# Optimization experiments

Hardware: AMD Instinct MI355X
Metric: run time of the kernel (lower is better)

Reference implementation:

```python
import jax, jax.numpy as jnp
import numpy as np

N_HEADS = 16
D_MODEL = 1024
D_K = 64
D_V = 64
LN_EPS = 1e-6


def setup_inputs() -> dict:
    key = jax.random.key(0)
    ks = jax.random.split(key, 16)
    B, L, D = 4, 512, D_MODEL
    s = 1.0 / np.sqrt(D)
    return {
        "q": jax.random.normal(ks[0], (B, L, D), jnp.float32),
        "k": jax.random.normal(ks[1], (B, L, D), jnp.float32),
        "v": jax.random.normal(ks[2], (B, L, D), jnp.float32),
        "bias": jax.random.normal(ks[3], (B, N_HEADS, L, L), jnp.float32),
        "graph_attn_bias": jax.random.normal(ks[4], (B, N_HEADS, L, L), jnp.float32),
        # projection weights stored as [in, out] (math-equivalent to torch Linear)
        "wq": jax.random.normal(ks[5], (D, N_HEADS * D_K), jnp.float32) * s,
        "bq": jnp.zeros((N_HEADS * D_K,), jnp.float32),
        "wk": jax.random.normal(ks[6], (D, N_HEADS * D_K), jnp.float32) * s,
        "bk": jnp.zeros((N_HEADS * D_K,), jnp.float32),
        "wv": jax.random.normal(ks[7], (D, N_HEADS * D_V), jnp.float32) * s,
        "bv": jnp.zeros((N_HEADS * D_V,), jnp.float32),
        "wo": jax.random.normal(ks[8], (N_HEADS * D_V, D), jnp.float32) * s,
        "bo": jnp.zeros((D,), jnp.float32),
        "ln_g": jnp.ones((D,), jnp.float32),
        "ln_b": jnp.zeros((D,), jnp.float32),
    }


def reference(q, k, v, bias, graph_attn_bias, wq, bq, wk, bk, wv, bv, wo, bo, ln_g, ln_b):
    B, Lq, D = q.shape
    H, dk, dv = N_HEADS, D_K, D_V
    residual = q
    # fused QKV projections, split heads -> [B, H, L, d]
    qh = (q @ wq + bq).reshape(B, Lq, H, dk).transpose(0, 2, 1, 3)
    kh = (k @ wk + bk).reshape(B, k.shape[1], H, dk).transpose(0, 2, 1, 3)
    vh = (v @ wv + bv).reshape(B, v.shape[1], H, dv).transpose(0, 2, 1, 3)
    # graph scaled dot-product attention: scores + mask bias + structural bias
    scores = jnp.einsum("bhqd,bhkd->bhqk", qh / np.sqrt(dk).astype(qh.dtype), kh)
    scores = scores + bias + graph_attn_bias
    weights = jax.nn.softmax(scores, axis=-1)
    ctx = jnp.einsum("bhqk,bhkd->bhqd", weights, vh)  # [B,H,Lq,dv]
    ctx = ctx.transpose(0, 2, 1, 3).reshape(B, Lq, H * dv)
    out = ctx @ wo + bo + residual
    # LayerNorm(eps=1e-6)
    mu = jnp.mean(out, axis=-1, keepdims=True)
    var = jnp.var(out, axis=-1, keepdims=True)
    out = (out - mu) * jax.lax.rsqrt(var + LN_EPS) * ln_g + ln_b
    return out
```

## Files before the change

kernel.cpp:

```cpp
#include <hip/hip_runtime.h>

#define D_MODEL 1024
#define N_HEADS 16
#define DK 64
#define LSEQ 512
#define BATCH 4
#define M_ROWS (BATCH * LSEQ)

typedef unsigned short ushort_t;
typedef __attribute__((ext_vector_type(8))) short short8;
typedef __attribute__((ext_vector_type(4))) float floatx4;

__device__ __forceinline__ float bf2f(unsigned short u) {
    return __uint_as_float(((unsigned int)u) << 16);
}
__device__ __forceinline__ unsigned short f2bf(float f) {
    unsigned int u = __float_as_uint(f);
    u += 0x7fffu + ((u >> 16) & 1u);
    return (unsigned short)(u >> 16);
}

__global__ __launch_bounds__(256) void cast3_kernel(
    const float* __restrict__ a, const float* __restrict__ b,
    const float* __restrict__ c, ushort_t* __restrict__ oa,
    ushort_t* __restrict__ ob, ushort_t* __restrict__ oc, int n)
{
    const float* src = (blockIdx.y == 0) ? a : (blockIdx.y == 1) ? b : c;
    ushort_t* dst = (blockIdx.y == 0) ? oa : (blockIdx.y == 1) ? ob : oc;
    int i = (blockIdx.x * 256 + threadIdx.x) * 4;
    if (i + 3 < n) {
        float4 v = *(const float4*)(src + i);
        ushort4 o = make_ushort4(f2bf(v.x), f2bf(v.y), f2bf(v.z), f2bf(v.w));
        *(ushort4*)(dst + i) = o;
    }
}

__global__ __launch_bounds__(256) void transpose4_kernel(
    const float* __restrict__ w0, const float* __restrict__ w1,
    const float* __restrict__ w2, const float* __restrict__ w3,
    ushort_t* __restrict__ o0, ushort_t* __restrict__ o1,
    ushort_t* __restrict__ o2, ushort_t* __restrict__ o3)
{
    __shared__ float tile[32][33];
    const float* W = (blockIdx.z == 0) ? w0 : (blockIdx.z == 1) ? w1
                   : (blockIdx.z == 2) ? w2 : w3;
    ushort_t* O = (blockIdx.z == 0) ? o0 : (blockIdx.z == 1) ? o1
                : (blockIdx.z == 2) ? o2 : o3;
    const int tx = threadIdx.x & 31;
    const int ty = threadIdx.x >> 5;
    const int kbase = blockIdx.y * 32;
    const int nbase = blockIdx.x * 32;
    #pragma unroll
    for (int j = 0; j < 4; ++j)
        tile[ty + 8 * j][tx] = W[(size_t)(kbase + ty + 8 * j) * 1024 + nbase + tx];
    __syncthreads();
    #pragma unroll
    for (int j = 0; j < 4; ++j) {
        int n = nbase + ty + 8 * j;
        O[(size_t)n * 1024 + kbase + tx] = f2bf(tile[tx][ty + 8 * j]);
    }
}

template <bool OUT_BF16, bool ADD_BVEC, bool ADD_RES>
__device__ __forceinline__ void gemm_bt_body(
    const ushort_t* __restrict__ A, const ushort_t* __restrict__ Bt,
    const float* __restrict__ bvec, const float* __restrict__ res,
    void* __restrict__ outp, int N, int K, int kStart, int kEnd,
    int rowBase, int colBase, ushort_t* As, ushort_t* Bs)
{
    const int tid = threadIdx.x;
    const int l = tid & 63;
    const int w = tid >> 6;
    const int wave_m = w >> 1;
    const int wave_n = w & 1;

    const int srow8 = l >> 3;
    const int cgl = ((l & 7) + srow8) & 7;
    const ushort_t* gA0 = A  + (size_t)(rowBase + w * 16 + 0 + srow8) * K + cgl * 8;
    const ushort_t* gA1 = A  + (size_t)(rowBase + w * 16 + 8 + srow8) * K + cgl * 8;
    const ushort_t* gB0 = Bt + (size_t)(colBase + w * 16 + 0 + srow8) * K + cgl * 8;
    const ushort_t* gB1 = Bt + (size_t)(colBase + w * 16 + 8 + srow8) * K + cgl * 8;
    ushort_t* lA0 = As + w * 1024;
    ushort_t* lA1 = As + w * 1024 + 512;
    ushort_t* lB0 = Bs + w * 1024;
    ushort_t* lB1 = Bs + w * 1024 + 512;

    floatx4 acc[2][2];
    #pragma unroll
    for (int i = 0; i < 2; ++i)
        #pragma unroll
        for (int j = 0; j < 2; ++j)
            acc[i][j] = (floatx4){0.f, 0.f, 0.f, 0.f};

    const int fm = l & 15;
    const int fg = l >> 4;

    for (int k0 = kStart; k0 < kEnd; k0 += 64) {
        __builtin_amdgcn_global_load_lds(
            (const __attribute__((address_space(1))) void*)(gA0 + k0),
            (__attribute__((address_space(3))) void*)lA0, 16, 0, 0);
        __builtin_amdgcn_global_load_lds(
            (const __attribute__((address_space(1))) void*)(gA1 + k0),
            (__attribute__((address_space(3))) void*)lA1, 16, 0, 0);
        __builtin_amdgcn_global_load_lds(
            (const __attribute__((address_space(1))) void*)(gB0 + k0),
            (__attribute__((address_space(3))) void*)lB0, 16, 0, 0);
        __builtin_amdgcn_global_load_lds(
            (const __attribute__((address_space(1))) void*)(gB1 + k0),
            (__attribute__((address_space(3))) void*)lB1, 16, 0, 0);
        __syncthreads();

        short8 afrag[2][2], bfrag[2][2];
        #pragma unroll
        for (int mi = 0; mi < 2; ++mi)
            #pragma unroll
            for (int kt = 0; kt < 2; ++kt) {
                int p = ((kt * 4 + fg) - fm) & 7;
                afrag[mi][kt] = *(const short8*)
                    &As[(wave_m * 32 + mi * 16 + fm) * 64 + p * 8];
            }
        #pragma unroll
        for (int ni = 0; ni < 2; ++ni)
            #pragma unroll
            for (int kt = 0; kt < 2; ++kt) {
                int p = ((kt * 4 + fg) - fm) & 7;
                bfrag[ni][kt] = *(const short8*)
                    &Bs[(wave_n * 32 + ni * 16 + fm) * 64 + p * 8];
            }

        #pragma unroll
        for (int kt = 0; kt < 2; ++kt)
            #pragma unroll
            for (int mi = 0; mi < 2; ++mi)
                #pragma unroll
                for (int ni = 0; ni < 2; ++ni)
                    acc[mi][ni] = __builtin_amdgcn_mfma_f32_16x16x32_bf16(
                        afrag[mi][kt], bfrag[ni][kt], acc[mi][ni], 0, 0, 0);
        __syncthreads();
    }

    const int crow0 = rowBase + wave_m * 32 + fg * 4;
    const int ccol0 = colBase + wave_n * 32 + fm;
    #pragma unroll
    for (int mi = 0; mi < 2; ++mi) {
        #pragma unroll
        for (int ni = 0; ni < 2; ++ni) {
            const int col = ccol0 + ni * 16;
            const float bb = ADD_BVEC ? bvec[col] : 0.f;
            #pragma unroll
            for (int r = 0; r < 4; ++r) {
                const int row = crow0 + mi * 16 + r;
                float v = acc[mi][ni][r] + bb;
                if (ADD_RES) v += res[(size_t)row * N + col];
                if (OUT_BF16)
                    ((ushort_t*)outp)[(size_t)row * N + col] = f2bf(v);
                else
                    ((float*)outp)[(size_t)row * N + col] = v;
            }
        }
    }
}

__global__ __launch_bounds__(256) void gemm_qkv(
    const ushort_t* a0, const ushort_t* a1, const ushort_t* a2,
    const ushort_t* t0, const ushort_t* t1, const ushort_t* t2,
    const float* b0, const float* b1, const float* b2,
    ushort_t* o0, ushort_t* o1, ushort_t* o2)
{
    __shared__ ushort_t As[64 * 64];
    __shared__ ushort_t Bs[64 * 64];
    const int z = blockIdx.z;
    const ushort_t* A  = (z == 0) ? a0 : (z == 1) ? a1 : a2;
    const ushort_t* Bt = (z == 0) ? t0 : (z == 1) ? t1 : t2;
    const float* bv    = (z == 0) ? b0 : (z == 1) ? b1 : b2;
    ushort_t* o        = (z == 0) ? o0 : (z == 1) ? o1 : o2;
    gemm_bt_body<true, true, false>(A, Bt, bv, nullptr, o, D_MODEL, D_MODEL,
                                    0, D_MODEL,
                                    blockIdx.y * 64, blockIdx.x * 64, As, Bs);
}

__global__ __launch_bounds__(256) void gemm_out(
    const ushort_t* __restrict__ A, const ushort_t* __restrict__ Bt,
    const float* __restrict__ bvec, const float* __restrict__ res,
    float* __restrict__ out0, float* __restrict__ out1)
{
    __shared__ ushort_t As[64 * 64];
    __shared__ ushort_t Bs[64 * 64];
    if (blockIdx.z == 0)
        gemm_bt_body<false, true, true>(A, Bt, bvec, res, out0, D_MODEL,
                                        D_MODEL, 0, 512,
                                        blockIdx.y * 64, blockIdx.x * 64, As, Bs);
    else
        gemm_bt_body<false, false, false>(A, Bt, nullptr, nullptr, out1, D_MODEL,
                                          D_MODEL, 512, 1024,
                                          blockIdx.y * 64, blockIdx.x * 64, As, Bs);
}

__global__ __launch_bounds__(256, 4) void attn_mfma(
    const ushort_t* __restrict__ qh, const ushort_t* __restrict__ kh,
    const ushort_t* __restrict__ vh, const float* __restrict__ bias,
    const float* __restrict__ gbias, ushort_t* __restrict__ ctx)
{
    __shared__ __attribute__((aligned(16))) ushort_t Qs[16 * 72];
    __shared__ __attribute__((aligned(16))) ushort_t P[16 * 520];
    __shared__ float Vt[64 * 36];
    __shared__ float redm[4][16];
    __shared__ float reds[4][16];

    const int tid = threadIdx.x;
    const int l = tid & 63;
    const int w = tid >> 6;
    const int m = l & 15;
    const int g = l >> 4;

    const int bh = blockIdx.y;
    const int h = bh & (N_HEADS - 1);
    const int b = bh >> 4;
    const int q0 = blockIdx.x * 16;

    const ushort_t* Qg = qh + ((size_t)(b * LSEQ + q0)) * D_MODEL + h * DK;
    const ushort_t* Kg = kh + ((size_t)(b * LSEQ)) * D_MODEL + h * DK;
    const ushort_t* Vg = vh + ((size_t)(b * LSEQ)) * D_MODEL + h * DK;

    if (tid < 128) {
        int row = tid >> 3, seg = tid & 7;
        short8 t = *(const short8*)(Qg + (size_t)row * D_MODEL + seg * 8);
        *(short8*)&Qs[row * 72 + seg * 8] = t;
    }
    __syncthreads();

    short8 aq0 = *(const short8*)&Qs[m * 72 + g * 8];
    short8 aq1 = *(const short8*)&Qs[m * 72 + g * 8 + 32];

    floatx4 acc[8];
    #pragma unroll
    for (int it = 0; it < 8; ++it) {
        const int kb = it * 64 + w * 16;
        const ushort_t* kr = Kg + (size_t)(kb + m) * D_MODEL + g * 8;
        short8 bk0 = *(const short8*)kr;
        short8 bk1 = *(const short8*)(kr + 32);
        floatx4 a = (floatx4){0.f, 0.f, 0.f, 0.f};
        a = __builtin_amdgcn_mfma_f32_16x16x32_bf16(aq0, bk0, a, 0, 0, 0);
        a = __builtin_amdgcn_mfma_f32_16x16x32_bf16(aq1, bk1, a, 0, 0, 0);
        acc[it] = a;
    }

    const float* bp = bias  + ((size_t)bh * LSEQ + q0) * LSEQ + w * 16 + m;
    const float* gp = gbias + ((size_t)bh * LSEQ + q0) * LSEQ + w * 16 + m;
    float bsum[8][4];
    #pragma unroll
    for (int it = 0; it < 8; ++it)
        #pragma unroll
        for (int r = 0; r < 4; ++r) {
            const size_t off = (size_t)(g * 4 + r) * LSEQ + it * 64;
            bsum[it][r] = bp[off] + gp[off];
        }
    #pragma unroll
    for (int it = 0; it < 8; ++it)
        #pragma unroll
        for (int r = 0; r < 4; ++r)
            acc[it][r] = acc[it][r] * 0.125f + bsum[it][r];

    float mx[4];
    #pragma unroll
    for (int r = 0; r < 4; ++r) {
        float pm = fmaxf(
            fmaxf(fmaxf(acc[0][r], acc[1][r]), fmaxf(acc[2][r], acc[3][r])),
            fmaxf(fmaxf(acc[4][r], acc[5][r]), fmaxf(acc[6][r], acc[7][r])));
        #pragma unroll
        for (int d = 1; d < 16; d <<= 1)
            pm = fmaxf(pm, __shfl_xor(pm, d, 64));
        mx[r] = pm;
    }
    if (m == 0) {
        #pragma unroll
        for (int r = 0; r < 4; ++r) redm[w][g * 4 + r] = mx[r];
    }
    __syncthreads();
    #pragma unroll
    for (int r = 0; r < 4; ++r)
        mx[r] = fmaxf(fmaxf(redm[0][g * 4 + r], redm[1][g * 4 + r]),
                      fmaxf(redm[2][g * 4 + r], redm[3][g * 4 + r]));

    float sm[4] = {0.f, 0.f, 0.f, 0.f};
    #pragma unroll
    for (int it = 0; it < 8; ++it)
        #pragma unroll
        for (int r = 0; r < 4; ++r) {
            float e = __expf(acc[it][r] - mx[r]);
            sm[r] += e;
            P[(g * 4 + r) * 520 + it * 64 + w * 16 + m] = f2bf(e);
        }
    #pragma unroll
    for (int r = 0; r < 4; ++r) {
        #pragma unroll
        for (int d = 1; d < 16; d <<= 1)
            sm[r] += __shfl_xor(sm[r], d, 64);
    }
    if (m == 0) {
        #pragma unroll
        for (int r = 0; r < 4; ++r) reds[w][g * 4 + r] = sm[r];
    }
    __syncthreads();
    float rinv[4];
    #pragma unroll
    for (int r = 0; r < 4; ++r)
        rinv[r] = 1.0f / (reds[0][g * 4 + r] + reds[1][g * 4 + r] +
                          reds[2][g * 4 + r] + reds[3][g * 4 + r]);

    floatx4 oacc = (floatx4){0.f, 0.f, 0.f, 0.f};
    const unsigned* VtD = (const unsigned*)Vt;

    for (int vt = 0; vt < 8; ++vt) {
        const int kv0 = vt * 64;
        __syncthreads();
        {
            const int kp = tid & 31, dg = tid >> 5;
            const ushort_t* vr = Vg + (size_t)(kv0 + 2 * kp) * D_MODEL + dg * 8;
            short8 r0 = *(const short8*)vr;
            short8 r1 = *(const short8*)(vr + D_MODEL);
            unsigned* vtp = (unsigned*)Vt;
            #pragma unroll
            for (int i = 0; i < 8; ++i) {
                unsigned dwv = (unsigned)(ushort_t)r0[i]
                             | ((unsigned)(ushort_t)r1[i] << 16);
                vtp[(dg * 8 + i) * 36 + kp] = dwv;
            }
        }
        __syncthreads();
        #pragma unroll
        for (int kt = 0; kt < 2; ++kt) {
            short8 pf = *(const short8*)&P[(size_t)m * 520 + kv0 + kt * 32 + g * 8];
            short8 vf = *(const short8*)&VtD[(w * 16 + m) * 36 + kt * 16 + g * 4];
            oacc = __builtin_amdgcn_mfma_f32_16x16x32_bf16(pf, vf, oacc, 0, 0, 0);
        }
    }

    {
        const int qrow0 = g * 4;
        const int dcol = w * 16 + m;
        ushort_t* cp = ctx + ((size_t)(b * LSEQ + q0 + qrow0)) * D_MODEL + h * DK + dcol;
        #pragma unroll
        for (int r = 0; r < 4; ++r)
            cp[(size_t)r * D_MODEL] = f2bf(oacc[r] * rinv[r]);
    }
}

__global__ __launch_bounds__(256) void ln_kernel(
    float* __restrict__ x, const float* __restrict__ part2,
    const float* __restrict__ g, const float* __restrict__ beta)
{
    const int row = blockIdx.x;
    float* xr = x + (size_t)row * D_MODEL;
    const float* pr = part2 + (size_t)row * D_MODEL;
    const int tid = threadIdx.x;

    float v[4];
    float s = 0.f, sq = 0.f;
    #pragma unroll
    for (int j = 0; j < 4; ++j) {
        v[j] = xr[tid + 256 * j] + pr[tid + 256 * j];
        s += v[j];
        sq += v[j] * v[j];
    }
    __shared__ float rs[256], rq[256];
    rs[tid] = s;
    rq[tid] = sq;
    __syncthreads();
    for (int st = 128; st > 0; st >>= 1) {
        if (tid < st) { rs[tid] += rs[tid + st]; rq[tid] += rq[tid + st]; }
        __syncthreads();
    }
    const float mean = rs[0] * (1.0f / D_MODEL);
    const float var = rq[0] * (1.0f / D_MODEL) - mean * mean;
    const float rinv = rsqrtf(var + 1e-6f);
    #pragma unroll
    for (int j = 0; j < 4; ++j) {
        int n = tid + 256 * j;
        xr[n] = (v[j] - mean) * rinv * g[n] + beta[n];
    }
}

extern "C" void kernel_launch(void* const* d_in, const int* in_sizes, int n_in,
                              void* d_out, int out_size, void* d_ws, size_t ws_size,
                              hipStream_t stream)
{
    const float* q     = (const float*)d_in[0];
    const float* k     = (const float*)d_in[1];
    const float* v     = (const float*)d_in[2];
    const float* bias  = (const float*)d_in[3];
    const float* gbias = (const float*)d_in[4];
    const float* wq    = (const float*)d_in[5];
    const float* bq    = (const float*)d_in[6];
    const float* wk    = (const float*)d_in[7];
    const float* bk    = (const float*)d_in[8];
    const float* wv    = (const float*)d_in[9];
    const float* bv    = (const float*)d_in[10];
    const float* wo    = (const float*)d_in[11];
    const float* bo    = (const float*)d_in[12];
    const float* ln_g  = (const float*)d_in[13];
    const float* ln_b  = (const float*)d_in[14];

    const size_t MB = 1u << 20;
    char* wsb = (char*)d_ws;
    ushort_t* vb   = (ushort_t*)(wsb + 0 * MB);
    ushort_t* wqb  = (ushort_t*)(wsb + 4 * MB);
    ushort_t* wkb  = (ushort_t*)(wsb + 6 * MB);
    ushort_t* wvb  = (ushort_t*)(wsb + 8 * MB);
    ushort_t* wob  = (ushort_t*)(wsb + 10 * MB);
    ushort_t* qhb  = (ushort_t*)(wsb + 12 * MB);
    ushort_t* khb  = (ushort_t*)(wsb + 16 * MB);
    ushort_t* vhb  = (ushort_t*)(wsb + 20 * MB);
    ushort_t* ctxb = (ushort_t*)(wsb + 24 * MB);
    float* out1 = (float*)(wsb + 12 * MB);
    ushort_t* qb = (ushort_t*)d_out;
    ushort_t* kb = (ushort_t*)d_out + (size_t)M_ROWS * D_MODEL;
    float* outp = (float*)d_out;

    const int NELEM = M_ROWS * D_MODEL;

    cast3_kernel<<<dim3(NELEM / 1024, 3), 256, 0, stream>>>(
        q, k, v, qb, kb, vb, NELEM);
    transpose4_kernel<<<dim3(32, 32, 4), 256, 0, stream>>>(
        wq, wk, wv, wo, wqb, wkb, wvb, wob);

    dim3 gqkv(D_MODEL / 64, M_ROWS / 64, 3);
    gemm_qkv<<<gqkv, 256, 0, stream>>>(
        qb, kb, vb, wqb, wkb, wvb, bq, bk, bv, qhb, khb, vhb);

    dim3 ablk(LSEQ / 16, BATCH * N_HEADS);
    attn_mfma<<<ablk, 256, 0, stream>>>(qhb, khb, vhb, bias, gbias, ctxb);

    dim3 gout(D_MODEL / 64, M_ROWS / 64, 2);
    gemm_out<<<gout, 256, 0, stream>>>(ctxb, wob, bo, q, outp, out1);

    ln_kernel<<<M_ROWS, 256, 0, stream>>>(outp, out1, ln_g, ln_b);
}
```

Baseline: 270.2 us.

## Stage bias tiles via async global-to-LDS loads and double-buffer V transposes

The attention kernel now prefetches all K fragments into registers up front. It issues global_load_lds DMA for the bias and graph-bias tiles into a 64KB shared buffer so those loads overlap the QK MFMAs, and then reads the biases from LDS. P and a double-buffered transposed V tile reuse the same shared region, with new strides, and the next V rows are prefetched into registers while MFMAs consume the current buffer, which removes one barrier per iteration. Occupancy drops: launch bounds go from 4 to 2 blocks and LDS use rises to about 67KB per block, so fewer waves are available to hide latency.

```diff
diff --git a/kernel.cpp b/kernel.cpp
--- a/kernel.cpp
+++ b/kernel.cpp
@@ -196,16 +196,24 @@
                                           blockIdx.y * 64, blockIdx.x * 64, As, Bs);
 }
 
-__global__ __launch_bounds__(256, 4) void attn_mfma(
+#define P_STRIDE 536
+#define VT_STRIDE 44
+#define VT_OFF 17408
+#define VT_BYTES 11264
+
+__global__ __launch_bounds__(256, 2) void attn_mfma(
     const ushort_t* __restrict__ qh, const ushort_t* __restrict__ kh,
     const ushort_t* __restrict__ vh, const float* __restrict__ bias,
     const float* __restrict__ gbias, ushort_t* __restrict__ ctx)
 {
+    __shared__ __attribute__((aligned(16))) unsigned char smem[65536];
     __shared__ __attribute__((aligned(16))) ushort_t Qs[16 * 72];
-    __shared__ __attribute__((aligned(16))) ushort_t P[16 * 520];
-    __shared__ float Vt[64 * 36];
     __shared__ float redm[4][16];
     __shared__ float reds[4][16];
+
+    float* biasL  = (float*)smem;
+    float* gbiasL = (float*)(smem + 32768);
+    ushort_t* Pl  = (ushort_t*)smem;
 
     const int tid = threadIdx.x;
     const int l = tid & 63;
@@ -232,34 +240,53 @@
     short8 aq0 = *(const short8*)&Qs[m * 72 + g * 8];
     short8 aq1 = *(const short8*)&Qs[m * 72 + g * 8 + 32];
 
+    short8 bk0[8], bk1[8];
+    #pragma unroll
+    for (int it = 0; it < 8; ++it) {
+        const ushort_t* kr = Kg + (size_t)(it * 64 + w * 16 + m) * D_MODEL + g * 8;
+        bk0[it] = *(const short8*)kr;
+        bk1[it] = *(const short8*)(kr + 32);
+    }
+
+    {
+        const float* bb = bias  + ((size_t)bh * LSEQ + q0) * LSEQ;
+        const float* gb = gbias + ((size_t)bh * LSEQ + q0) * LSEQ;
+        #pragma unroll
+        for (int i = 0; i < 4; ++i) {
+            const int row = w * 4 + i;
+            const size_t roff = (size_t)row * LSEQ;
+            #pragma unroll
+            for (int c = 0; c < 2; ++c) {
+                __builtin_amdgcn_global_load_lds(
+                    (const __attribute__((address_space(1))) void*)(bb + roff + c * 256 + l * 4),
+                    (__attribute__((address_space(3))) void*)(biasL + row * 512 + c * 256),
+                    16, 0, 0);
+                __builtin_amdgcn_global_load_lds(
+                    (const __attribute__((address_space(1))) void*)(gb + roff + c * 256 + l * 4),
+                    (__attribute__((address_space(3))) void*)(gbiasL + row * 512 + c * 256),
+                    16, 0, 0);
+            }
+        }
+    }
+
     floatx4 acc[8];
     #pragma unroll
     for (int it = 0; it < 8; ++it) {
-        const int kb = it * 64 + w * 16;
-        const ushort_t* kr = Kg + (size_t)(kb + m) * D_MODEL + g * 8;
-        short8 bk0 = *(const short8*)kr;
-        short8 bk1 = *(const short8*)(kr + 32);
         floatx4 a = (floatx4){0.f, 0.f, 0.f, 0.f};
-        a = __builtin_amdgcn_mfma_f32_16x16x32_bf16(aq0, bk0, a, 0, 0, 0);
-        a = __builtin_amdgcn_mfma_f32_16x16x32_bf16(aq1, bk1, a, 0, 0, 0);
+        a = __builtin_amdgcn_mfma_f32_16x16x32_bf16(aq0, bk0[it], a, 0, 0, 0);
+        a = __builtin_amdgcn_mfma_f32_16x16x32_bf16(aq1, bk1[it], a, 0, 0, 0);
         acc[it] = a;
     }
 
-    const float* bp = bias  + ((size_t)bh * LSEQ + q0) * LSEQ + w * 16 + m;
-    const float* gp = gbias + ((size_t)bh * LSEQ + q0) * LSEQ + w * 16 + m;
-    float bsum[8][4];
+    __syncthreads();
+
     #pragma unroll
     for (int it = 0; it < 8; ++it)
         #pragma unroll
         for (int r = 0; r < 4; ++r) {
-            const size_t off = (size_t)(g * 4 + r) * LSEQ + it * 64;
-            bsum[it][r] = bp[off] + gp[off];
-        }
-    #pragma unroll
-    for (int it = 0; it < 8; ++it)
-        #pragma unroll
-        for (int r = 0; r < 4; ++r)
-            acc[it][r] = acc[it][r] * 0.125f + bsum[it][r];
+            const int idx = (g * 4 + r) * 512 + it * 64 + w * 16 + m;
+            acc[it][r] = acc[it][r] * 0.125f + (biasL[idx] + gbiasL[idx]);
+        }
 
     float mx[4];
     #pragma unroll
@@ -289,7 +316,7 @@
         for (int r = 0; r < 4; ++r) {
             float e = __expf(acc[it][r] - mx[r]);
             sm[r] += e;
-            P[(g * 4 + r) * 520 + it * 64 + w * 16 + m] = f2bf(e);
+            Pl[(g * 4 + r) * P_STRIDE + it * 64 + w * 16 + m] = f2bf(e);
         }
     #pragma unroll
     for (int r = 0; r < 4; ++r) {
@@ -309,29 +336,29 @@
                           reds[2][g * 4 + r] + reds[3][g * 4 + r]);
 
     floatx4 oacc = (floatx4){0.f, 0.f, 0.f, 0.f};
-    const unsigned* VtD = (const unsigned*)Vt;
-
+    const int kp = tid & 31, dg = tid >> 5;
+    const ushort_t* vb0 = Vg + (size_t)(2 * kp) * D_MODEL + dg * 8;
+    short8 r0 = *(const short8*)vb0;
+    short8 r1 = *(const short8*)(vb0 + D_MODEL);
+
+    #pragma unroll
     for (int vt = 0; vt < 8; ++vt) {
-        const int kv0 = vt * 64;
+        unsigned* vtp = (unsigned*)(smem + VT_OFF + (vt & 1) * VT_BYTES);
+        #pragma unroll
+        for (int i = 0; i < 8; ++i)
+            vtp[(dg * 8 + i) * VT_STRIDE + kp] =
+                (unsigned)(ushort_t)r0[i] | ((unsigned)(ushort_t)r1[i] << 16);
         __syncthreads();
-        {
-            const int kp = tid & 31, dg = tid >> 5;
-            const ushort_t* vr = Vg + (size_t)(kv0 + 2 * kp) * D_MODEL + dg * 8;
-            short8 r0 = *(const short8*)vr;
-            short8 r1 = *(const short8*)(vr + D_MODEL);
-            unsigned* vtp = (unsigned*)Vt;
-            #pragma unroll
-            for (int i = 0; i < 8; ++i) {
-                unsigned dwv = (unsigned)(ushort_t)r0[i]
-                             | ((unsigned)(ushort_t)r1[i] << 16);
-                vtp[(dg * 8 + i) * 36 + kp] = dwv;
-            }
-        }
-        __syncthreads();
+        if (vt < 7) {
+            const ushort_t* vr = vb0 + (size_t)((vt + 1) * 64) * D_MODEL;
+            r0 = *(const short8*)vr;
+            r1 = *(const short8*)(vr + D_MODEL);
+        }
+        const unsigned* VtDb = (const unsigned*)(smem + VT_OFF + (vt & 1) * VT_BYTES);
         #pragma unroll
         for (int kt = 0; kt < 2; ++kt) {
-            short8 pf = *(const short8*)&P[(size_t)m * 520 + kv0 + kt * 32 + g * 8];
-            short8 vf = *(const short8*)&VtD[(w * 16 + m) * 36 + kt * 16 + g * 4];
+            short8 pf = *(const short8*)&Pl[(size_t)m * P_STRIDE + vt * 64 + kt * 32 + g * 8];
+            short8 vf = *(const short8*)&VtDb[(w * 16 + m) * VT_STRIDE + kt * 16 + g * 4];
             oacc = __builtin_amdgcn_mfma_f32_16x16x32_bf16(pf, vf, oacc, 0, 0, 0);
         }
     }
```

Measured after the change: 273.1 us. About the same (+1.1%).

## Write V projection pre-transposed per head and drop in-kernel V transpose

Applied to the files above, without the earlier changes.

The QKV GEMM epilogue now writes the V projection in a per-(batch, head) transposed layout [d][L]. The attention kernel can then load V fragments directly from global memory, removing the per-tile shared-memory transpose and its two barriers per iteration. The attention kernel also raises its occupancy hint to 5 blocks per unit and reduces unrolling of the score and PV loops to 2 to save registers. The trade-off is that the PV loop now issues uncached global loads for V, and the QK loop exposes more load latency.

```diff
diff --git a/kernel.cpp b/kernel.cpp
--- a/kernel.cpp
+++ b/kernel.cpp
@@ -61,7 +61,7 @@
     }
 }
 
-template <bool OUT_BF16, bool ADD_BVEC, bool ADD_RES>
+template <bool OUT_BF16, bool ADD_BVEC, bool ADD_RES, bool OUT_VT>
 __device__ __forceinline__ void gemm_bt_body(
     const ushort_t* __restrict__ A, const ushort_t* __restrict__ Bt,
     const float* __restrict__ bvec, const float* __restrict__ res,
@@ -147,15 +147,27 @@
         for (int ni = 0; ni < 2; ++ni) {
             const int col = ccol0 + ni * 16;
             const float bb = ADD_BVEC ? bvec[col] : 0.f;
-            #pragma unroll
-            for (int r = 0; r < 4; ++r) {
-                const int row = crow0 + mi * 16 + r;
-                float v = acc[mi][ni][r] + bb;
-                if (ADD_RES) v += res[(size_t)row * N + col];
-                if (OUT_BF16)
-                    ((ushort_t*)outp)[(size_t)row * N + col] = f2bf(v);
-                else
-                    ((float*)outp)[(size_t)row * N + col] = v;
+            if (OUT_VT) {
+                const int row0 = crow0 + mi * 16;
+                ushort4 pk;
+                pk.x = f2bf(acc[mi][ni][0] + bb);
+                pk.y = f2bf(acc[mi][ni][1] + bb);
+                pk.z = f2bf(acc[mi][ni][2] + bb);
+                pk.w = f2bf(acc[mi][ni][3] + bb);
+                const size_t base =
+                    ((size_t)((row0 >> 9) * 16 + (col >> 6)) * 64 + (col & 63)) * 512;
+                *(ushort4*)&((ushort_t*)outp)[base + (row0 & 511)] = pk;
+            } else {
+                #pragma unroll
+                for (int r = 0; r < 4; ++r) {
+                    const int row = crow0 + mi * 16 + r;
+                    float v = acc[mi][ni][r] + bb;
+                    if (ADD_RES) v += res[(size_t)row * N + col];
+                    if (OUT_BF16)
+                        ((ushort_t*)outp)[(size_t)row * N + col] = f2bf(v);
+                    else
+                        ((float*)outp)[(size_t)row * N + col] = v;
+                }
             }
         }
     }
@@ -170,13 +182,19 @@
     __shared__ ushort_t As[64 * 64];
     __shared__ ushort_t Bs[64 * 64];
     const int z = blockIdx.z;
-    const ushort_t* A  = (z == 0) ? a0 : (z == 1) ? a1 : a2;
-    const ushort_t* Bt = (z == 0) ? t0 : (z == 1) ? t1 : t2;
-    const float* bv    = (z == 0) ? b0 : (z == 1) ? b1 : b2;
-    ushort_t* o        = (z == 0) ? o0 : (z == 1) ? o1 : o2;
-    gemm_bt_body<true, true, false>(A, Bt, bv, nullptr, o, D_MODEL, D_MODEL,
-                                    0, D_MODEL,
-                                    blockIdx.y * 64, blockIdx.x * 64, As, Bs);
+    if (z == 2) {
+        gemm_bt_body<true, true, false, true>(a2, t2, b2, nullptr, o2, D_MODEL,
+                                              D_MODEL, 0, D_MODEL,
+                                              blockIdx.y * 64, blockIdx.x * 64, As, Bs);
+    } else {
+        const ushort_t* A  = (z == 0) ? a0 : a1;
+        const ushort_t* Bt = (z == 0) ? t0 : t1;
+        const float* bv    = (z == 0) ? b0 : b1;
+        ushort_t* o        = (z == 0) ? o0 : o1;
+        gemm_bt_body<true, true, false, false>(A, Bt, bv, nullptr, o, D_MODEL,
+                                               D_MODEL, 0, D_MODEL,
+                                               blockIdx.y * 64, blockIdx.x * 64, As, Bs);
+    }
 }
 
 __global__ __launch_bounds__(256) void gemm_out(
@@ -187,23 +205,24 @@
     __shared__ ushort_t As[64 * 64];
     __shared__ ushort_t Bs[64 * 64];
     if (blockIdx.z == 0)
-        gemm_bt_body<false, true, true>(A, Bt, bvec, res, out0, D_MODEL,
-                                        D_MODEL, 0, 512,
-                                        blockIdx.y * 64, blockIdx.x * 64, As, Bs);
+        gemm_bt_body<false, true, true, false>(A, Bt, bvec, res, out0, D_MODEL,
+                                               D_MODEL, 0, 512,
+                                               blockIdx.y * 64, blockIdx.x * 64, As, Bs);
     else
-        gemm_bt_body<false, false, false>(A, Bt, nullptr, nullptr, out1, D_MODEL,
-                                          D_MODEL, 512, 1024,
-                                          blockIdx.y * 64, blockIdx.x * 64, As, Bs);
-}
-
-__global__ __launch_bounds__(256, 4) void attn_mfma(
+        gemm_bt_body<false, false, false, false>(A, Bt, nullptr, nullptr, out1, D_MODEL,
+                                                 D_MODEL, 512, 1024,
+                                                 blockIdx.y * 64, blockIdx.x * 64, As, Bs);
+}
+
+#define P_STRIDE 520
+
+__global__ __launch_bounds__(256, 5) void attn_mfma(
     const ushort_t* __restrict__ qh, const ushort_t* __restrict__ kh,
-    const ushort_t* __restrict__ vh, const float* __restrict__ bias,
+    const ushort_t* __restrict__ vt, const float* __restrict__ bias,
     const float* __restrict__ gbias, ushort_t* __restrict__ ctx)
 {
     __shared__ __attribute__((aligned(16))) ushort_t Qs[16 * 72];
-    __shared__ __attribute__((aligned(16))) ushort_t P[16 * 520];
-    __shared__ float Vt[64 * 36];
+    __shared__ __attribute__((aligned(16))) ushort_t P[16 * P_STRIDE];
     __shared__ float redm[4][16];
     __shared__ float reds[4][16];
 
@@ -220,7 +239,7 @@
 
     const ushort_t* Qg = qh + ((size_t)(b * LSEQ + q0)) * D_MODEL + h * DK;
     const ushort_t* Kg = kh + ((size_t)(b * LSEQ)) * D_MODEL + h * DK;
-    const ushort_t* Vg = vh + ((size_t)(b * LSEQ)) * D_MODEL + h * DK;
+    const ushort_t* Vt_g = vt + (size_t)bh * DK * LSEQ;
 
     if (tid < 128) {
         int row = tid >> 3, seg = tid & 7;
@@ -233,7 +252,7 @@
     short8 aq1 = *(const short8*)&Qs[m * 72 + g * 8 + 32];
 
     floatx4 acc[8];
-    #pragma unroll
+    #pragma unroll 2
     for (int it = 0; it < 8; ++it) {
         const int kb = it * 64 + w * 16;
         const ushort_t* kr = Kg + (size_t)(kb + m) * D_MODEL + g * 8;
@@ -289,7 +308,7 @@
         for (int r = 0; r < 4; ++r) {
             float e = __expf(acc[it][r] - mx[r]);
             sm[r] += e;
-            P[(g * 4 + r) * 520 + it * 64 + w * 16 + m] = f2bf(e);
+            P[(g * 4 + r) * P_STRIDE + it * 64 + w * 16 + m] = f2bf(e);
         }
     #pragma unroll
     for (int r = 0; r < 4; ++r) {
@@ -309,29 +328,15 @@
                           reds[2][g * 4 + r] + reds[3][g * 4 + r]);
 
     floatx4 oacc = (floatx4){0.f, 0.f, 0.f, 0.f};
-    const unsigned* VtD = (const unsigned*)Vt;
-
-    for (int vt = 0; vt < 8; ++vt) {
-        const int kv0 = vt * 64;
-        __syncthreads();
-        {
-            const int kp = tid & 31, dg = tid >> 5;
-            const ushort_t* vr = Vg + (size_t)(kv0 + 2 * kp) * D_MODEL + dg * 8;
-            short8 r0 = *(const short8*)vr;
-            short8 r1 = *(const short8*)(vr + D_MODEL);
-            unsigned* vtp = (unsigned*)Vt;
-            #pragma unroll
-            for (int i = 0; i < 8; ++i) {
-                unsigned dwv = (unsigned)(ushort_t)r0[i]
-                             | ((unsigned)(ushort_t)r1[i] << 16);
-                vtp[(dg * 8 + i) * 36 + kp] = dwv;
-            }
-        }
-        __syncthreads();
+    const ushort_t* vrow = Vt_g + (size_t)(w * 16 + m) * LSEQ + g * 8;
+    const ushort_t* prow = &P[(size_t)m * P_STRIDE + g * 8];
+    #pragma unroll 2
+    for (int vtile = 0; vtile < 8; ++vtile) {
         #pragma unroll
         for (int kt = 0; kt < 2; ++kt) {
-            short8 pf = *(const short8*)&P[(size_t)m * 520 + kv0 + kt * 32 + g * 8];
-            short8 vf = *(const short8*)&VtD[(w * 16 + m) * 36 + kt * 16 + g * 4];
+            const int ko = vtile * 64 + kt * 32;
+            short8 pf = *(const short8*)(prow + ko);
+            short8 vf = *(const short8*)(vrow + ko);
             oacc = __builtin_amdgcn_mfma_f32_16x16x32_bf16(pf, vf, oacc, 0, 0, 0);
         }
     }
@@ -410,7 +415,7 @@
     ushort_t* wob  = (ushort_t*)(wsb + 10 * MB);
     ushort_t* qhb  = (ushort_t*)(wsb + 12 * MB);
     ushort_t* khb  = (ushort_t*)(wsb + 16 * MB);
-    ushort_t* vhb  = (ushort_t*)(wsb + 20 * MB);
+    ushort_t* vtb  = (ushort_t*)(wsb + 20 * MB);
     ushort_t* ctxb = (ushort_t*)(wsb + 24 * MB);
     float* out1 = (float*)(wsb + 12 * MB);
     ushort_t* qb = (ushort_t*)d_out;
@@ -426,10 +431,10 @@
 
     dim3 gqkv(D_MODEL / 64, M_ROWS / 64, 3);
     gemm_qkv<<<gqkv, 256, 0, stream>>>(
-        qb, kb, vb, wqb, wkb, wvb, bq, bk, bv, qhb, khb, vhb);
+        qb, kb, vb, wqb, wkb, wvb, bq, bk, bv, qhb, khb, vtb);
 
     dim3 ablk(LSEQ / 16, BATCH * N_HEADS);
-    attn_mfma<<<ablk, 256, 0, stream>>>(qhb, khb, vhb, bias, gbias, ctxb);
+    attn_mfma<<<ablk, 256, 0, stream>>>(qhb, khb, vtb, bias, gbias, ctxb);
 
     dim3 gout(D_MODEL / 64, M_ROWS / 64, 2);
     gemm_out<<<gout, 256, 0, stream>>>(ctxb, wob, bo, q, outp, out1);
```

Result: slower. 309.3 us (+14.5%).
